# Performance work log

Hardware: AMD Instinct MI355X
Metric: run time of the kernel (lower is better)

The kernel has to match this reference:

```python
import jax, jax.numpy as jnp
import numpy as np
from jax import lax

BZ = 1024; ROI = 116; DIM = 116; FLAT = ROI * DIM
TOPK = 8; TEMP = 0.07; ALPHA = 0.1; A_COEF = 0.9; BETA = 2; EPS = 1e-5


def _leaky(v):
    return jnp.where(v >= 0, v, 0.2 * v)


def _bn2d(h, g, b):
    # training-mode BatchNorm1d on [N, C] (biased variance)
    m = h.mean(0)
    v = h.var(0)
    return (h - m) * lax.rsqrt(v + EPS) * g + b


def setup_inputs():
    key = jax.random.key(0)
    ks = jax.random.split(key, 16)
    def w(k, shape, s=0.05):
        return jax.random.normal(k, shape, jnp.float32) * s
    return {
        "x": jax.random.normal(ks[0], (BZ, ROI, DIM), jnp.float32),
        "pseudo": jax.random.normal(ks[1], (BZ, ROI, DIM), jnp.float32),
        "ages": jax.random.randint(ks[2], (BZ,), 0, 80, jnp.int32),
        "genders": jax.random.randint(ks[3], (BZ,), 0, 2, jnp.int32),
        "site": jax.random.randint(ks[4], (BZ, 4), 0, 10, jnp.int32),
        "fc_p_w": w(ks[5], (ROI, ROI)), "fc_p_b": jnp.zeros((ROI,), jnp.float32),
        "proj_w1": w(ks[6], (FLAT, ROI), 0.01), "proj_b1": jnp.zeros((ROI,), jnp.float32),
        "proj_w2": w(ks[7], (ROI, ROI)), "proj_b2": jnp.zeros((ROI,), jnp.float32),
        "gcn_w1": w(ks[8], (DIM, ROI)), "gcn_b1": jnp.zeros((ROI,), jnp.float32),
        "gcn_w2": w(ks[9], (ROI, ROI)), "gcn_b2": jnp.zeros((ROI,), jnp.float32),
        "gcn1_w": w(ks[10], (ROI, ROI)), "gcn1_b": jnp.zeros((ROI,), jnp.float32),
        "gcn2_w1": w(ks[11], (ROI, 64)), "gcn2_b1": jnp.zeros((64,), jnp.float32),
        "gcn2_w2": w(ks[12], (64, 8)), "gcn2_b2": jnp.zeros((8,), jnp.float32),
        "bn1_g": jnp.ones((ROI,), jnp.float32), "bn1_b": jnp.zeros((ROI,), jnp.float32),
        "bn2_g": jnp.ones((ROI,), jnp.float32), "bn2_b": jnp.zeros((ROI,), jnp.float32),
        "bn3_g": jnp.ones((ROI,), jnp.float32), "bn3_b": jnp.zeros((ROI,), jnp.float32),
    }


def _forward(x, pseudo, fc_p_w, fc_p_b, proj_w1, proj_b1, proj_w2, proj_b2,
             gcn_w1, gcn_b1, gcn_w2, gcn_b2, gcn1_w, gcn1_b,
             gcn2_w1, gcn2_b1, gcn2_w2, gcn2_b2,
             bn1_g, bn1_b, bn2_g, bn2_b, bn3_g, bn3_b,
             pos_idx, neg_idx, cond):
    bz = x.shape[0]
    pseudo = _leaky(pseudo @ fc_p_w + fc_p_b)
    x = x + pseudo                               # [bz, roi, dim]
    xf = x.reshape(bz, -1)                       # [bz, roi*dim]
    # contrastive head: Linear-ReLU-Linear, L2-normalize, cosine sim / temp
    p = jnp.maximum(xf @ proj_w1 + proj_b1, 0.0) @ proj_w2 + proj_b2
    pn = p / jnp.linalg.norm(p, axis=1, keepdims=True)
    sim = (pn @ pn.T) / TEMP                     # [bz, bz]
    sflat = sim.ravel()
    # -log(exp(pos)/(exp(pos)+exp(neg))) == softplus(neg - pos), truncated pairing
    loss = jnp.mean(jax.nn.softplus(sflat[neg_idx] - sflat[pos_idx]))
    sim_n = (sim - sim.min()) / (sim.max() - sim.min())
    # adjacency build: original does it in detached numpy -> stop_gradient
    xd = lax.stop_gradient(xf)
    sd = lax.stop_gradient(sim_n)
    sq = jnp.sum(xd * xd, axis=1)
    d2 = jnp.maximum(sq[:, None] + sq[None, :] - 2.0 * (xd @ xd.T), 0.0)
    fsim = jnp.exp(-ALPHA * jnp.sqrt(d2))
    total = fsim * (1.0 - sd) + sd
    dist = total * jnp.where(cond, A_COEF, 1.0 - A_COEF)
    vals, idxs = lax.top_k(dist, TOPK)           # row-wise top-8
    adj = jnp.zeros((bz, bz), jnp.float32).at[jnp.arange(bz)[:, None], idxs].set(vals)
    # GCN stack with flattened-feature message passing
    h = (adj @ xf).reshape(bz, ROI, DIM)
    h = _leaky(h @ gcn_w1 + gcn_b1) @ gcn_w2 + gcn_b2
    h = _bn2d(h.reshape(bz * ROI, -1), bn1_g, bn1_b).reshape(bz, ROI, -1)
    h = (adj @ h.reshape(bz, -1)).reshape(bz, ROI, -1)
    h = _leaky(h @ gcn1_w + gcn1_b)
    h = _bn2d(h.reshape(bz * ROI, -1), bn2_g, bn2_b).reshape(bz, ROI, -1)
    h = (adj @ h.reshape(bz, -1)).reshape(bz, ROI, -1)
    h = _leaky(_leaky(h @ gcn2_w1 + gcn2_b1) @ gcn2_w2 + gcn2_b2)  # [bz, roi, 8]
    # bn3: BatchNorm1d on [N, C=roi, L=8] -> per-channel over (N, L)
    m = h.mean((0, 2), keepdims=True)
    v = h.var((0, 2), keepdims=True)
    h = (h - m) * lax.rsqrt(v + EPS) * bn3_g[None, :, None] + bn3_b[None, :, None]
    return h, loss


def _masks(ages, genders, site):
    labels = np.asarray(site).argmax(1)
    eq = (labels[:, None] == labels[None, :]).ravel()
    pos_idx = np.nonzero(eq)[0]
    neg_idx = np.nonzero(~eq)[0]
    m = min(pos_idx.size, neg_idx.size)
    ag = np.asarray(ages); gd = np.asarray(genders)
    cond = (np.abs(ag[:, None] - ag[None, :]) <= BETA) & (gd[:, None] == gd[None, :])
    return jnp.asarray(pos_idx[:m]), jnp.asarray(neg_idx[:m]), jnp.asarray(cond)


def reference(x, pseudo, ages, genders, site, fc_p_w, fc_p_b, proj_w1, proj_b1,
              proj_w2, proj_b2, gcn_w1, gcn_b1, gcn_w2, gcn_b2, gcn1_w, gcn1_b,
              gcn2_w1, gcn2_b1, gcn2_w2, gcn2_b2, bn1_g, bn1_b, bn2_g, bn2_b,
              bn3_g, bn3_b):
    pos_idx, neg_idx, cond = _masks(ages, genders, site)
    return _forward(x, pseudo, fc_p_w, fc_p_b, proj_w1, proj_b1, proj_w2, proj_b2,
                    gcn_w1, gcn_b1, gcn_w2, gcn_b2, gcn1_w, gcn1_b,
                    gcn2_w1, gcn2_b1, gcn2_w2, gcn2_b2,
                    bn1_g, bn1_b, bn2_g, bn2_b, bn3_g, bn3_b,
                    pos_idx, neg_idx, cond)
```

## Files before the change

### kernel.cpp

```cpp
#include <hip/hip_runtime.h>
#include <math.h>

#define ROIN 116
#define NBZ 1024
#define LDF 128
#define SROW (ROIN*LDF)
#define NROWS (NBZ*ROIN)
#define ALPHA 0.1f
#define ACOEF 0.9f
#define BETAC 2
#define EPSBN 1e-5f
#define PZ 29
#define PCH 512
#define W1LD SROW
#define GX2 928
#define GX45 1856
#define GRAMZ 16
#define GRAMKS 928
#define NTRI 36

typedef __attribute__((ext_vector_type(8))) short bf16x8;
typedef __attribute__((ext_vector_type(4))) float f32x4;

__device__ __forceinline__ float leakyf(float v){ return v >= 0.f ? v : 0.2f*v; }

__device__ __forceinline__ short f2bf(float f){
    unsigned u = __builtin_bit_cast(unsigned, f);
    unsigned r = u + 0x7fffu + ((u >> 16) & 1u);
    return (short)(r >> 16);
}
__device__ __forceinline__ float bf2f(short h){
    unsigned u = ((unsigned)(unsigned short)h) << 16;
    return __builtin_bit_cast(float, u);
}

__global__ void wt_conv(const float* __restrict__ W, short* __restrict__ hi,
                        short* __restrict__ lo, int K, int N)
{
    int idx = blockIdx.x * 256 + threadIdx.x;
    int n = idx >> 7, k = idx & 127;
    float v = (n < N && k < K) ? W[(size_t)k * N + n] : 0.f;
    short h = f2bf(v);
    hi[idx] = h;
    lo[idx] = f2bf(v - bf2f(h));
}

__global__ void wt1_conv(const float* __restrict__ W, short* __restrict__ hi,
                         short* __restrict__ lo)
{
    int idx = blockIdx.x * 256 + threadIdx.x;
    int n = idx / W1LD, k = idx - n * W1LD;
    int r = k >> 7, d = k & 127;
    float v = (n < ROIN && d < ROIN) ? W[(size_t)(r * ROIN + d) * ROIN + n] : 0.f;
    short h = f2bf(v);
    hi[idx] = h;
    lo[idx] = f2bf(v - bf2f(h));
}

template<int EPI, int XTRA, bool PADK>
__global__ __launch_bounds__(512) void mfma_gemm_w(
    const float* __restrict__ A, const short* __restrict__ wt_hi,
    const short* __restrict__ wt_lo, const float* __restrict__ bias,
    const float* __restrict__ X, float* __restrict__ C,
    short* __restrict__ bfout, float* __restrict__ rsq, float* __restrict__ statp,
    int LDA, int LDC)
{
    __shared__ short whi[128][136];
    __shared__ short wlo[128][136];
    __shared__ float st[(XTRA == 2) ? 8 : 1][2][128];
    const int tid = threadIdx.x;
    {
        int r = tid >> 2, q = tid & 3;
        const short* sh = wt_hi + r * 128 + q * 32;
        const short* sl = wt_lo + r * 128 + q * 32;
        #pragma unroll
        for (int i = 0; i < 4; ++i) {
            *(bf16x8*)(&whi[r][q * 32 + i * 8]) = *(const bf16x8*)(sh + i * 8);
            *(bf16x8*)(&wlo[r][q * 32 + i * 8]) = *(const bf16x8*)(sl + i * 8);
        }
    }
    __syncthreads();
    const int wave = tid >> 6, lane = tid & 63;
    const int m0 = blockIdx.x * 128 + wave * 16;
    const int rl = lane & 15, g = lane >> 4;
    const float* Arow = A + (size_t)(m0 + rl) * LDA;
    float av[4][8];
    #pragma unroll
    for (int s = 0; s < 4; ++s) {
        const int kk = s * 32 + g * 8;
        if (PADK || kk + 8 <= ROIN) {
            float4 p = *(const float4*)(Arow + kk);
            float4 q = *(const float4*)(Arow + kk + 4);
            av[s][0]=p.x; av[s][1]=p.y; av[s][2]=p.z; av[s][3]=p.w;
            av[s][4]=q.x; av[s][5]=q.y; av[s][6]=q.z; av[s][7]=q.w;
        } else if (kk + 4 <= ROIN) {
            float4 p = *(const float4*)(Arow + kk);
            av[s][0]=p.x; av[s][1]=p.y; av[s][2]=p.z; av[s][3]=p.w;
            av[s][4]=0.f; av[s][5]=0.f; av[s][6]=0.f; av[s][7]=0.f;
        } else {
            #pragma unroll
            for (int j = 0; j < 8; ++j) av[s][j] = 0.f;
        }
    }
    f32x4 acc[8];
    #pragma unroll
    for (int nf = 0; nf < 8; ++nf) acc[nf] = (f32x4){0.f,0.f,0.f,0.f};
    #pragma unroll
    for (int s = 0; s < 4; ++s) {
        const int kk = s * 32 + g * 8;
        bf16x8 ah, al;
        #pragma unroll
        for (int j = 0; j < 8; ++j) {
            short h = f2bf(av[s][j]); ah[j] = h;
            al[j] = f2bf(av[s][j] - bf2f(h));
        }
        #pragma unroll
        for (int nf = 0; nf < 8; ++nf) {
            const bf16x8 bh = *(const bf16x8*)(&whi[nf * 16 + rl][kk]);
            const bf16x8 bl = *(const bf16x8*)(&wlo[nf * 16 + rl][kk]);
            acc[nf] = __builtin_amdgcn_mfma_f32_16x16x32_bf16(ah, bh, acc[nf], 0, 0, 0);
            acc[nf] = __builtin_amdgcn_mfma_f32_16x16x32_bf16(al, bh, acc[nf], 0, 0, 0);
            acc[nf] = __builtin_amdgcn_mfma_f32_16x16x32_bf16(ah, bl, acc[nf], 0, 0, 0);
        }
    }
    const int cm = g * 4;
    float rq[4] = {0.f, 0.f, 0.f, 0.f};
    bf16x8 bfv[4];
    #pragma unroll
    for (int nf = 0; nf < 8; ++nf) {
        int n = nf * 16 + rl;
        float c1 = 0.f, c2 = 0.f;
        float bb = (n < ROIN) ? bias[n] : 0.f;
        #pragma unroll
        for (int j = 0; j < 4; ++j) {
            int m = m0 + cm + j;
            size_t idx = (size_t)m * LDC + n;
            float v = 0.f;
            if (n < ROIN) {
                v = acc[nf][j] + bb;
                if (EPI == 3) v = leakyf(v);
                else if (EPI == 4) v = X[(size_t)m * LDA + n] + leakyf(v);
            }
            if (n < LDC) C[idx] = v;
            if (XTRA == 1) { bfv[j][nf] = f2bf(v); rq[j] += v * v; }
            if (XTRA == 2) { c1 += v; c2 += v * v; }
        }
        if (XTRA == 2) {
            c1 += __shfl_xor(c1, 16); c1 += __shfl_xor(c1, 32);
            c2 += __shfl_xor(c2, 16); c2 += __shfl_xor(c2, 32);
            if (lane < 16) { st[wave][0][n & 127] = c1; st[wave][1][n & 127] = c2; }
        }
    }
    if (XTRA == 1) {
        #pragma unroll
        for (int j = 0; j < 4; ++j)
            *(bf16x8*)(&bfout[(size_t)(m0 + cm + j) * LDF + rl * 8]) = bfv[j];
        #pragma unroll
        for (int j = 0; j < 4; ++j) {
            rq[j] += __shfl_xor(rq[j], 1);
            rq[j] += __shfl_xor(rq[j], 2);
            rq[j] += __shfl_xor(rq[j], 4);
            rq[j] += __shfl_xor(rq[j], 8);
        }
        if (rl == 0) {
            #pragma unroll
            for (int j = 0; j < 4; ++j) rsq[m0 + cm + j] = rq[j];
        }
    }
    if (XTRA == 2) {
        __syncthreads();
        if (tid < 232) {
            int sel = tid < 116 ? 0 : 1;
            int c = sel ? tid - 116 : tid;
            float s = 0.f;
            #pragma unroll
            for (int wv = 0; wv < 8; ++wv) s += st[wv][sel][c];
            statp[(size_t)(sel * 116 + c) * GX2 + blockIdx.x] = s;
        }
    }
}

template<int EPI, int XTRA, bool FOLD>
__global__ __launch_bounds__(512, 4) void mfma_gemm_wg(
    const float* __restrict__ vals, const int* __restrict__ idxs,
    const float* __restrict__ feat, const float* __restrict__ sb,
    const float* __restrict__ tb,
    const short* __restrict__ wt_hi, const short* __restrict__ wt_lo,
    const float* __restrict__ bias, float* __restrict__ C,
    float* __restrict__ statp)
{
    __shared__ short whi[128][136];
    __shared__ short wlo[128][136];
    __shared__ float st[(XTRA == 2) ? 8 : 1][2][128];
    const int tid = threadIdx.x;
    {
        int r = tid >> 2, q = tid & 3;
        const short* sh = wt_hi + r * 128 + q * 32;
        const short* sl = wt_lo + r * 128 + q * 32;
        #pragma unroll
        for (int i = 0; i < 4; ++i) {
            *(bf16x8*)(&whi[r][q * 32 + i * 8]) = *(const bf16x8*)(sh + i * 8);
            *(bf16x8*)(&wlo[r][q * 32 + i * 8]) = *(const bf16x8*)(sl + i * 8);
        }
    }
    __syncthreads();
    const int wave = tid >> 6, lane = tid & 63;
    const int m0 = blockIdx.x * 128 + wave * 16;
    const int rl = lane & 15, g = lane >> 4;
    const int m = m0 + rl;
    const unsigned bz = (unsigned)m / 116u;
    const int r = m - (int)bz * 116;
    float vv[8]; const float4* fp[8];
    #pragma unroll
    for (int k = 0; k < 8; ++k) {
        vv[k] = vals[bz * 8 + k];
        int ixk = idxs[bz * 8 + k];
        fp[k] = (const float4*)(feat + ((size_t)ixk * 116 + r) * 128);
    }
    float wsum = 0.f;
    if (FOLD) {
        #pragma unroll
        for (int k = 0; k < 8; ++k) wsum += vv[k];
    }
    f32x4 acc[8];
    #pragma unroll
    for (int nf = 0; nf < 8; ++nf) acc[nf] = (f32x4){0.f,0.f,0.f,0.f};
    float4 xp[8], xq[8];
    const int fb = g * 2;
    #pragma unroll
    for (int k = 0; k < 8; ++k) xp[k] = fp[k][fb];
    #pragma unroll
    for (int k = 0; k < 8; ++k) xq[k] = fp[k][fb + 1];
    #pragma unroll
    for (int s = 0; s < 4; ++s) {
        const int kk = s * 32 + g * 8;
        float4 P = {0.f,0.f,0.f,0.f}, Q = {0.f,0.f,0.f,0.f};
        #pragma unroll
        for (int k = 0; k < 8; ++k) {
            P.x = fmaf(vv[k], xp[k].x, P.x); P.y = fmaf(vv[k], xp[k].y, P.y);
            P.z = fmaf(vv[k], xp[k].z, P.z); P.w = fmaf(vv[k], xp[k].w, P.w);
            Q.x = fmaf(vv[k], xq[k].x, Q.x); Q.y = fmaf(vv[k], xq[k].y, Q.y);
            Q.z = fmaf(vv[k], xq[k].z, Q.z); Q.w = fmaf(vv[k], xq[k].w, Q.w);
        }
        if (s < 3) {
            const int fn = fb + (s + 1) * 8;
            #pragma unroll
            for (int k = 0; k < 8; ++k) xp[k] = fp[k][fn];
            #pragma unroll
            for (int k = 0; k < 8; ++k) xq[k] = fp[k][fn + 1];
        }
        float av[8] = {P.x, P.y, P.z, P.w, Q.x, Q.y, Q.z, Q.w};
        if (FOLD) {
            #pragma unroll
            for (int j = 0; j < 8; ++j) {
                int c = kk + j;
                av[j] = (c < ROIN) ? sb[c] * av[j] + wsum * tb[c] : 0.f;
            }
        }
        bf16x8 ah, al;
        #pragma unroll
        for (int j = 0; j < 8; ++j) {
            short h = f2bf(av[j]); ah[j] = h;
            al[j] = f2bf(av[j] - bf2f(h));
        }
        __builtin_amdgcn_s_setprio(1);
        #pragma unroll
        for (int nf = 0; nf < 8; ++nf) {
            const bf16x8 bh = *(const bf16x8*)(&whi[nf * 16 + rl][kk]);
            const bf16x8 bl = *(const bf16x8*)(&wlo[nf * 16 + rl][kk]);
            acc[nf] = __builtin_amdgcn_mfma_f32_16x16x32_bf16(ah, bh, acc[nf], 0, 0, 0);
            acc[nf] = __builtin_amdgcn_mfma_f32_16x16x32_bf16(al, bh, acc[nf], 0, 0, 0);
            acc[nf] = __builtin_amdgcn_mfma_f32_16x16x32_bf16(ah, bl, acc[nf], 0, 0, 0);
        }
        __builtin_amdgcn_s_setprio(0);
    }
    const int cm = g * 4;
    #pragma unroll
    for (int nf = 0; nf < 8; ++nf) {
        int n = nf * 16 + rl;
        float c1 = 0.f, c2 = 0.f;
        float bb = (n < ROIN) ? bias[n] : 0.f;
        #pragma unroll
        for (int j = 0; j < 4; ++j) {
            int mm = m0 + cm + j;
            float v = 0.f;
            if (n < ROIN) {
                v = acc[nf][j] + bb;
                if (EPI == 3) v = leakyf(v);
            }
            C[(size_t)mm * LDF + n] = v;
            if (XTRA == 2) { c1 += v; c2 += v * v; }
        }
        if (XTRA == 2) {
            c1 += __shfl_xor(c1, 16); c1 += __shfl_xor(c1, 32);
            c2 += __shfl_xor(c2, 16); c2 += __shfl_xor(c2, 32);
            if (lane < 16) { st[wave][0][n & 127] = c1; st[wave][1][n & 127] = c2; }
        }
    }
    if (XTRA == 2) {
        __syncthreads();
        if (tid < 232) {
            int sel = tid < 116 ? 0 : 1;
            int c = sel ? tid - 116 : tid;
            float s = 0.f;
            #pragma unroll
            for (int wv = 0; wv < 8; ++wv) s += st[wv][sel][c];
            statp[(size_t)(sel * 116 + c) * GX2 + blockIdx.x] = s;
        }
    }
}

__global__ __launch_bounds__(256) void mfma_gemm45_wg(
    const float* __restrict__ vals, const int* __restrict__ idxs,
    const float* __restrict__ feat, const float* __restrict__ sb,
    const float* __restrict__ tb,
    const short* __restrict__ w5h, const short* __restrict__ w5l,
    const float* __restrict__ b5,
    const short* __restrict__ w6h, const short* __restrict__ w6l,
    const float* __restrict__ b6,
    float* __restrict__ C)
{
    __shared__ short s5h[64][136], s5l[64][136];
    __shared__ short s6h[16][136], s6l[16][136];
    __shared__ float c1s[4][16][76];
    const int tid = threadIdx.x;
    {
        int r = tid >> 2, q = tid & 3;
        const short* sh = w5h + r * 128 + q * 32;
        const short* sl = w5l + r * 128 + q * 32;
        #pragma unroll
        for (int i = 0; i < 4; ++i) {
            *(bf16x8*)(&s5h[r][q * 32 + i * 8]) = *(const bf16x8*)(sh + i * 8);
            *(bf16x8*)(&s5l[r][q * 32 + i * 8]) = *(const bf16x8*)(sl + i * 8);
        }
        if (tid < 64) {
            int r6 = tid >> 2, q6 = tid & 3;
            const short* sh6 = w6h + r6 * 128 + q6 * 32;
            const short* sl6 = w6l + r6 * 128 + q6 * 32;
            #pragma unroll
            for (int i = 0; i < 4; ++i) {
                *(bf16x8*)(&s6h[r6][q6 * 32 + i * 8]) = *(const bf16x8*)(sh6 + i * 8);
                *(bf16x8*)(&s6l[r6][q6 * 32 + i * 8]) = *(const bf16x8*)(sl6 + i * 8);
            }
        }
    }
    __syncthreads();
    const int wave = tid >> 6, lane = tid & 63;
    const int m0 = blockIdx.x * 64 + wave * 16;
    const int rl = lane & 15, g = lane >> 4;
    const int m = m0 + rl;
    const unsigned bz = (unsigned)m / 116u;
    const int r = m - (int)bz * 116;
    float vv[8]; const float4* fp[8];
    #pragma unroll
    for (int k = 0; k < 8; ++k) {
        vv[k] = vals[bz * 8 + k];
        int ixk = idxs[bz * 8 + k];
        fp[k] = (const float4*)(feat + ((size_t)ixk * 116 + r) * 128);
    }
    float wsum = 0.f;
    #pragma unroll
    for (int k = 0; k < 8; ++k) wsum += vv[k];
    f32x4 acc[4];
    #pragma unroll
    for (int nf = 0; nf < 4; ++nf) acc[nf] = (f32x4){0.f,0.f,0.f,0.f};
    float4 xp[8], xq[8];
    const int fb = g * 2;
    #pragma unroll
    for (int k = 0; k < 8; ++k) xp[k] = fp[k][fb];
    #pragma unroll
    for (int k = 0; k < 8; ++k) xq[k] = fp[k][fb + 1];
    #pragma unroll
    for (int s = 0; s < 4; ++s) {
        const int kk = s * 32 + g * 8;
        float4 P = {0.f,0.f,0.f,0.f}, Q = {0.f,0.f,0.f,0.f};
        #pragma unroll
        for (int k = 0; k < 8; ++k) {
            P.x = fmaf(vv[k], xp[k].x, P.x); P.y = fmaf(vv[k], xp[k].y, P.y);
            P.z = fmaf(vv[k], xp[k].z, P.z); P.w = fmaf(vv[k], xp[k].w, P.w);
            Q.x = fmaf(vv[k], xq[k].x, Q.x); Q.y = fmaf(vv[k], xq[k].y, Q.y);
            Q.z = fmaf(vv[k], xq[k].z, Q.z); Q.w = fmaf(vv[k], xq[k].w, Q.w);
        }
        if (s < 3) {
            const int fn = fb + (s + 1) * 8;
            #pragma unroll
            for (int k = 0; k < 8; ++k) xp[k] = fp[k][fn];
            #pragma unroll
            for (int k = 0; k < 8; ++k) xq[k] = fp[k][fn + 1];
        }
        float av[8] = {P.x, P.y, P.z, P.w, Q.x, Q.y, Q.z, Q.w};
        #pragma unroll
        for (int j = 0; j < 8; ++j) {
            int c = kk + j;
            av[j] = (c < ROIN) ? sb[c] * av[j] + wsum * tb[c] : 0.f;
        }
        bf16x8 ah, al;
        #pragma unroll
        for (int j = 0; j < 8; ++j) {
            short h = f2bf(av[j]); ah[j] = h;
            al[j] = f2bf(av[j] - bf2f(h));
        }
        __builtin_amdgcn_s_setprio(1);
        #pragma unroll
        for (int nf = 0; nf < 4; ++nf) {
            const bf16x8 bh = *(const bf16x8*)(&s5h[nf * 16 + rl][kk]);
            const bf16x8 bl = *(const bf16x8*)(&s5l[nf * 16 + rl][kk]);
            acc[nf] = __builtin_amdgcn_mfma_f32_16x16x32_bf16(ah, bh, acc[nf], 0, 0, 0);
            acc[nf] = __builtin_amdgcn_mfma_f32_16x16x32_bf16(al, bh, acc[nf], 0, 0, 0);
            acc[nf] = __builtin_amdgcn_mfma_f32_16x16x32_bf16(ah, bl, acc[nf], 0, 0, 0);
        }
        __builtin_amdgcn_s_setprio(0);
    }
    const int cm = g * 4;
    #pragma unroll
    for (int nf = 0; nf < 4; ++nf) {
        int n = nf * 16 + rl;
        float bb = b5[n];
        #pragma unroll
        for (int j = 0; j < 4; ++j)
            c1s[wave][cm + j][n] = leakyf(acc[nf][j] + bb);
    }
    f32x4 acc2 = {0.f,0.f,0.f,0.f};
    #pragma unroll
    for (int s = 0; s < 2; ++s) {
        const int kk = s * 32 + g * 8;
        float4 p = *(const float4*)(&c1s[wave][rl][kk]);
        float4 q = *(const float4*)(&c1s[wave][rl][kk + 4]);
        float a2[8] = {p.x, p.y, p.z, p.w, q.x, q.y, q.z, q.w};
        bf16x8 ah, al;
        #pragma unroll
        for (int j = 0; j < 8; ++j) {
            short h = f2bf(a2[j]); ah[j] = h;
            al[j] = f2bf(a2[j] - bf2f(h));
        }
        const bf16x8 bh = *(const bf16x8*)(&s6h[rl][kk]);
        const bf16x8 bl = *(const bf16x8*)(&s6l[rl][kk]);
        acc2 = __builtin_amdgcn_mfma_f32_16x16x32_bf16(ah, bh, acc2, 0, 0, 0);
        acc2 = __builtin_amdgcn_mfma_f32_16x16x32_bf16(al, bh, acc2, 0, 0, 0);
        acc2 = __builtin_amdgcn_mfma_f32_16x16x32_bf16(ah, bl, acc2, 0, 0, 0);
    }
    if (rl < 8) {
        float bb = b6[rl];
        #pragma unroll
        for (int j = 0; j < 4; ++j) {
            float v = leakyf(acc2[j] + bb);
            C[(size_t)(m0 + cm + j) * 8 + rl] = v;
        }
    }
}

__global__ void bn_final_st(const float* __restrict__ statp, const float* __restrict__ g,
                            const float* __restrict__ bta, float* __restrict__ sb,
                            float* __restrict__ tb)
{
    int c = blockIdx.x, tid = threadIdx.x;
    float a1 = 0.f, a2 = 0.f;
    for (int i = tid; i < GX2; i += 256) {
        a1 += statp[(size_t)c * GX2 + i];
        a2 += statp[(size_t)(116 + c) * GX2 + i];
    }
    __shared__ float r1[256], r2[256];
    r1[tid] = a1; r2[tid] = a2; __syncthreads();
    for (int off = 128; off > 0; off >>= 1) {
        if (tid < off) { r1[tid] += r1[tid + off]; r2[tid] += r2[tid + off]; }
        __syncthreads();
    }
    if (tid == 0) {
        float mean = r1[0] / (float)NROWS;
        float var = r2[0] / (float)NROWS - mean * mean;
        float rstd = 1.f / sqrtf(var + EPSBN);
        float s = rstd * g[c];
        sb[c] = s;
        tb[c] = bta[c] - mean * s;
    }
}

__global__ void sq_reduce(const float* __restrict__ rsq, float* __restrict__ sq)
{
    int i = blockIdx.x * 256 + threadIdx.x;
    if (i >= NBZ) return;
    const float* p = rsq + (size_t)i * ROIN;
    float s = 0.f;
    #pragma unroll 4
    for (int r = 0; r < ROIN; ++r) s += p[r];
    sq[i] = s;
}

__global__ __launch_bounds__(256) void mfma_proj1(
    const float* __restrict__ A, const short* __restrict__ wt_hi,
    const short* __restrict__ wt_lo, float* __restrict__ part)
{
    const int wave = threadIdx.x >> 6, lane = threadIdx.x & 63;
    const int m0 = blockIdx.x * 64 + wave * 16;
    const int rl = lane & 15, g = lane >> 4;
    const int kbase = blockIdx.z * PCH;
    const float* Arow = A + (size_t)(m0 + rl) * SROW;
    f32x4 acc[8];
    #pragma unroll
    for (int nf = 0; nf < 8; ++nf) acc[nf] = (f32x4){0.f,0.f,0.f,0.f};
    for (int s = 0; s < 16; ++s) {
        const int kk = kbase + s * 32 + g * 8;
        float4 p = *(const float4*)(Arow + kk);
        float4 q = *(const float4*)(Arow + kk + 4);
        float av[8] = {p.x, p.y, p.z, p.w, q.x, q.y, q.z, q.w};
        bf16x8 ah, al;
        #pragma unroll
        for (int j = 0; j < 8; ++j) {
            short h = f2bf(av[j]); ah[j] = h;
            al[j] = f2bf(av[j] - bf2f(h));
        }
        #pragma unroll
        for (int nf = 0; nf < 8; ++nf) {
            size_t boff = (size_t)(nf * 16 + rl) * W1LD + kk;
            bf16x8 bh = *(const bf16x8*)(wt_hi + boff);
            bf16x8 bl = *(const bf16x8*)(wt_lo + boff);
            acc[nf] = __builtin_amdgcn_mfma_f32_16x16x32_bf16(ah, bh, acc[nf], 0, 0, 0);
            acc[nf] = __builtin_amdgcn_mfma_f32_16x16x32_bf16(al, bh, acc[nf], 0, 0, 0);
            acc[nf] = __builtin_amdgcn_mfma_f32_16x16x32_bf16(ah, bl, acc[nf], 0, 0, 0);
        }
    }
    float* Cb = part + (size_t)blockIdx.z * NBZ * ROIN;
    const int cm = g * 4;
    #pragma unroll
    for (int nf = 0; nf < 8; ++nf) {
        int n = nf * 16 + rl;
        if (n < ROIN) {
            #pragma unroll
            for (int j = 0; j < 4; ++j)
                Cb[(size_t)(m0 + cm + j) * ROIN + n] = acc[nf][j];
        }
    }
}

__global__ void proj_reduce(const float* __restrict__ ppart,
                            const float* __restrict__ bias, float* __restrict__ t1)
{
    int e = blockIdx.x * 256 + threadIdx.x;
    if (e >= NBZ * ROIN) return;
    int n = e % ROIN;
    float s = 0.f;
    for (int z = 0; z < PZ; ++z) s += ppart[(size_t)z * NBZ * ROIN + e];
    t1[e] = fmaxf(s + bias[n], 0.f);
}

__global__ __launch_bounds__(256) void gemm_nt_sym(
    const float* __restrict__ A, float* __restrict__ C, int M, int K, float scale)
{
    if ((int)blockIdx.y < (int)blockIdx.x) return;
    __shared__ float As[16][65];
    __shared__ float Bs[16][65];
    const int tid = threadIdx.x;
    const int m0 = blockIdx.x * 64;
    const int n0 = blockIdx.y * 64;
    const int tm4 = (tid >> 4) * 4;
    const int tn4 = (tid & 15) * 4;
    const int rA  = tid >> 2;
    const int kbA = (tid & 3) * 4;
    float acc[4][4] = {};
    for (int kt = 0; kt < K; kt += 16) {
        int kg = kt + kbA;
        if (kg + 4 <= K) {
            float4 va = *(const float4*)(A + (size_t)(m0 + rA) * K + kg);
            As[kbA + 0][rA] = va.x; As[kbA + 1][rA] = va.y;
            As[kbA + 2][rA] = va.z; As[kbA + 3][rA] = va.w;
            float4 vb = *(const float4*)(A + (size_t)(n0 + rA) * K + kg);
            Bs[kbA + 0][rA] = vb.x; Bs[kbA + 1][rA] = vb.y;
            Bs[kbA + 2][rA] = vb.z; Bs[kbA + 3][rA] = vb.w;
        } else {
            #pragma unroll
            for (int kk = 0; kk < 4; ++kk) {
                int kgg = kg + kk;
                As[kbA + kk][rA] = (kgg < K) ? A[(size_t)(m0 + rA) * K + kgg] : 0.f;
                Bs[kbA + kk][rA] = (kgg < K) ? A[(size_t)(n0 + rA) * K + kgg] : 0.f;
            }
        }
        __syncthreads();
        #pragma unroll
        for (int k = 0; k < 16; ++k) {
            float a[4], b[4];
            #pragma unroll
            for (int i = 0; i < 4; ++i) a[i] = As[k][tm4 + i];
            #pragma unroll
            for (int j = 0; j < 4; ++j) b[j] = Bs[k][tn4 + j];
            #pragma unroll
            for (int i = 0; i < 4; ++i)
                #pragma unroll
                for (int j = 0; j < 4; ++j)
                    acc[i][j] = fmaf(a[i], b[j], acc[i][j]);
        }
        __syncthreads();
    }
    #pragma unroll
    for (int i = 0; i < 4; ++i) {
        int m = m0 + tm4 + i;
        #pragma unroll
        for (int j = 0; j < 4; ++j) {
            int n = n0 + tn4 + j;
            float v = acc[i][j] * scale;
            C[(size_t)m * M + n] = v;
            C[(size_t)n * M + m] = v;
        }
    }
}

__global__ __launch_bounds__(256) void gram_mfma(
    const short* __restrict__ Xh, float* __restrict__ gpart)
{
    const int id = blockIdx.x;
    const int wg = (id & 7) * 72 + (id >> 3);
    const int z = wg / 36;
    const int tri = wg - z * 36;
    int bx = 0;
    #pragma unroll
    for (int b = 1; b < 8; ++b) {
        int base = b * 8 - (b * (b - 1)) / 2;
        if (base <= tri) bx = b;
    }
    const int by = tri - (bx * 8 - (bx * (bx - 1)) / 2) + bx;
    const int k0 = z * GRAMKS;
    const int wave = threadIdx.x >> 6, lane = threadIdx.x & 63;
    const int wr = wave >> 1, wc = wave & 1;
    const int row = lane & 15, koff = (lane >> 4) * 8;
    const short* Ap[4]; const short* Bp[4];
    #pragma unroll
    for (int i = 0; i < 4; ++i) {
        Ap[i] = Xh + (size_t)(bx * 128 + wr * 64 + i * 16 + row) * SROW;
// ... 204 lines not shown
        float v = sim[f];
        if (eq[kk]) { if (r < m) posval[r] = v; r++; }
        else { long nr = (long)f - r; if (nr < m) negval[nr] = v; }
    }
}

__global__ void loss_part(const float* __restrict__ posval, const float* __restrict__ negval,
                          const int* __restrict__ iscal, float* __restrict__ lp)
{
    int m = iscal[1];
    int t = threadIdx.x, b = blockIdx.x;
    float s = 0.f;
    for (int k = b * 256 + t; k < m; k += 1024 * 256) {
        float d = negval[k] - posval[k];
        s += fmaxf(d, 0.f) + log1pf(expf(-fabsf(d)));
    }
    __shared__ float red[256];
    red[t] = s; __syncthreads();
    for (int off = 128; off > 0; off >>= 1) { if (t < off) red[t] += red[t + off]; __syncthreads(); }
    if (t == 0) lp[b] = red[0];
}

__global__ void loss_final(const float* __restrict__ lp, const int* __restrict__ iscal,
                           float* __restrict__ outp)
{
    int t = threadIdx.x;
    double s = 0.0;
    for (int k = t; k < 1024; k += 256) s += (double)lp[k];
    __shared__ double red[256];
    red[t] = s; __syncthreads();
    for (int off = 128; off > 0; off >>= 1) { if (t < off) red[t] += red[t + off]; __syncthreads(); }
    if (t == 0) {
        int m = iscal[1]; if (m < 1) m = 1;
        outp[0] = (float)(red[0] / (double)m);
    }
}

__global__ void topk8(const float* __restrict__ dist, float* __restrict__ topv, int* __restrict__ topi)
{
    int row = blockIdx.x, t = threadIdx.x;
    __shared__ float sv[1024];
    __shared__ float rv[256];
    __shared__ int   ri[256];
    for (int j = t; j < 1024; j += 256) sv[j] = dist[(size_t)row * 1024 + j];
    __syncthreads();
    for (int k = 0; k < 8; ++k) {
        float bv = -1e30f; int bi = 1 << 20;
        for (int j = t; j < 1024; j += 256) {
            float x = sv[j];
            if (x > bv || (x == bv && j < bi)) { bv = x; bi = j; }
        }
        rv[t] = bv; ri[t] = bi;
        __syncthreads();
        for (int s = 128; s > 0; s >>= 1) {
            if (t < s) {
                float ov = rv[t + s]; int oi = ri[t + s];
                if (ov > rv[t] || (ov == rv[t] && oi < ri[t])) { rv[t] = ov; ri[t] = oi; }
            }
            __syncthreads();
        }
        if (t == 0) { topv[row * 8 + k] = rv[0]; topi[row * 8 + k] = ri[0]; sv[ri[0]] = -1e30f; }
        __syncthreads();
    }
}

__global__ void bn3_k(const float* __restrict__ X, const float* __restrict__ g,
                      const float* __restrict__ bta, float* __restrict__ out)
{
    int c = blockIdx.x, t = threadIdx.x;
    float s = 0.f, s2 = 0.f;
    for (int k = t; k < 8192; k += 256) {
        int n = k >> 3, l = k & 7;
        float v = X[(size_t)n * 928 + c * 8 + l];
        s += v; s2 += v * v;
    }
    __shared__ float rs[256], rs2[256];
    rs[t] = s; rs2[t] = s2; __syncthreads();
    for (int off = 128; off > 0; off >>= 1) {
        if (t < off) { rs[t] += rs[t + off]; rs2[t] += rs2[t + off]; }
        __syncthreads();
    }
    __shared__ float sm, sr;
    if (t == 0) {
        float mean = rs[0] / 8192.f;
        float var = rs2[0] / 8192.f - mean * mean;
        sm = mean; sr = 1.f / sqrtf(var + EPSBN);
    }
    __syncthreads();
    float mean = sm, rstd = sr, gg = g[c], bb = bta[c];
    for (int k = t; k < 8192; k += 256) {
        int n = k >> 3, l = k & 7;
        size_t idx = (size_t)n * 928 + c * 8 + l;
        out[idx] = (X[idx] - mean) * rstd * gg + bb;
    }
}

extern "C" void kernel_launch(void* const* d_in, const int* in_sizes, int n_in,
                              void* d_out, int out_size, void* d_ws, size_t ws_size,
                              hipStream_t stream)
{
    const float* x        = (const float*)d_in[0];
    const float* pseudo   = (const float*)d_in[1];
    const int*   ages     = (const int*)d_in[2];
    const int*   genders  = (const int*)d_in[3];
    const int*   site     = (const int*)d_in[4];
    const float* fc_p_w   = (const float*)d_in[5];
    const float* fc_p_b   = (const float*)d_in[6];
    const float* proj_w1  = (const float*)d_in[7];
    const float* proj_b1  = (const float*)d_in[8];
    const float* proj_w2  = (const float*)d_in[9];
    const float* proj_b2  = (const float*)d_in[10];
    const float* gcn_w1   = (const float*)d_in[11];
    const float* gcn_b1   = (const float*)d_in[12];
    const float* gcn_w2   = (const float*)d_in[13];
    const float* gcn_b2   = (const float*)d_in[14];
    const float* gcn1_w   = (const float*)d_in[15];
    const float* gcn1_b   = (const float*)d_in[16];
    const float* gcn2_w1  = (const float*)d_in[17];
    const float* gcn2_b1  = (const float*)d_in[18];
    const float* gcn2_w2  = (const float*)d_in[19];
    const float* gcn2_b2  = (const float*)d_in[20];
    const float* bn1_g    = (const float*)d_in[21];
    const float* bn1_b    = (const float*)d_in[22];
    const float* bn2_g    = (const float*)d_in[23];
    const float* bn2_b    = (const float*)d_in[24];
    const float* bn3_g    = (const float*)d_in[25];
    const float* bn3_b    = (const float*)d_in[26];
    float* dout = (float*)d_out;

    char* w = (char*)d_ws;
    size_t off = 0;
    auto carve = [&](size_t bytes) { char* p = w + off; off = (off + bytes + 255) & ~(size_t)255; return p; };
    float* xf     = (float*)carve((size_t)NROWS * LDF * 4);
    float* hA     = (float*)carve((size_t)NROWS * LDF * 4);
    float* hB     = (float*)carve((size_t)NROWS * LDF * 4);
    float* G      = (float*)carve(1048576u * 4);
    float* simb   = (float*)carve(1048576u * 4);
    float* t1     = (float*)carve((size_t)NBZ * ROIN * 4);
    float* pbuf   = (float*)carve((size_t)NBZ * ROIN * 4);
    float* sq     = (float*)carve(4096);
    float* rsq    = (float*)carve((size_t)NROWS * 4);
    int*   labels = (int*)carve(4096);
    int*   rowcnt = (int*)carve(4096);
    int*   rowoff = (int*)carve(4096);
    int*   iscal  = (int*)carve(256);
    float* fscal  = (float*)carve(256);
    float* posval = (float*)carve(524288u * 4);
    float* negval = (float*)carve(524288u * 4);
    float* lpart  = (float*)carve(4096);
    float* mmpart = (float*)carve(4096);
    float* topv   = (float*)carve(32768);
    int*   topi   = (int*)carve(32768);
    float* statp  = (float*)carve((size_t)232 * GX2 * 4);
    float* sbA    = (float*)carve(512);
    float* tbA    = (float*)carve(512);
    float* sbB    = (float*)carve(512);
    float* tbB    = (float*)carve(512);
    short* wt1_hi = (short*)carve((size_t)128 * W1LD * 2);
    short* wt1_lo = (short*)carve((size_t)128 * W1LD * 2);
    short* wts    = (short*)carve((size_t)7 * 2 * 16384 * 2);
    float* ppart  = hA;
    float* gpart  = hA;
    short* xfh    = (short*)((char*)hB + (16u << 20));

    auto wt_hi = [&](int i) { return wts + (size_t)i * 2 * 16384; };
    auto wt_lo = [&](int i) { return wts + (size_t)i * 2 * 16384 + 16384; };

    wt1_conv<<<(128 * W1LD) / 256, 256, 0, stream>>>(proj_w1, wt1_hi, wt1_lo);
    wt_conv<<<64, 256, 0, stream>>>(fc_p_w,   wt_hi(0), wt_lo(0), 116, 116);
    wt_conv<<<64, 256, 0, stream>>>(proj_w2,  wt_hi(1), wt_lo(1), 116, 116);
    wt_conv<<<64, 256, 0, stream>>>(gcn_w1,   wt_hi(2), wt_lo(2), 116, 116);
    wt_conv<<<64, 256, 0, stream>>>(gcn_w2,   wt_hi(3), wt_lo(3), 116, 116);
    wt_conv<<<64, 256, 0, stream>>>(gcn1_w,   wt_hi(4), wt_lo(4), 116, 116);
    wt_conv<<<64, 256, 0, stream>>>(gcn2_w1,  wt_hi(5), wt_lo(5), 116, 64);
    wt_conv<<<64, 256, 0, stream>>>(gcn2_w2,  wt_hi(6), wt_lo(6), 64, 8);

    mfma_gemm_w<4, 1, false><<<GX2, 512, 0, stream>>>(pseudo, wt_hi(0), wt_lo(0), fc_p_b, x, xf,
                                                      xfh, rsq, nullptr, ROIN, LDF);
    sq_reduce<<<4, 256, 0, stream>>>(rsq, sq);

    mfma_proj1<<<dim3(16, 1, PZ), 256, 0, stream>>>(xf, wt1_hi, wt1_lo, ppart);
    proj_reduce<<<(NBZ * ROIN + 255) / 256, 256, 0, stream>>>(ppart, proj_b1, t1);
    mfma_gemm_w<1, 0, false><<<8, 512, 0, stream>>>(t1, wt_hi(1), wt_lo(1), proj_b2, nullptr, pbuf,
                                                    nullptr, nullptr, nullptr, ROIN, ROIN);
    rownorm<<<NBZ, 128, 0, stream>>>(pbuf);

    gemm_nt_sym<<<dim3(16, 16, 1), 256, 0, stream>>>(pbuf, simb, NBZ, ROIN, 1.f / 0.07f);

    labels_k<<<4, 256, 0, stream>>>(site, labels);
    rowcnt_k<<<4, 256, 0, stream>>>(labels, rowcnt);
    scan_k<<<1, 1024, 0, stream>>>(rowcnt, rowoff, iscal);
    pair_scatter<<<NBZ, 256, 0, stream>>>(labels, rowoff, iscal, simb, posval, negval);
    loss_part<<<1024, 256, 0, stream>>>(posval, negval, iscal, lpart);
    loss_final<<<1, 256, 0, stream>>>(lpart, iscal, dout + (size_t)NBZ * ROIN * 8);

    minmax_part<<<512, 256, 0, stream>>>(simb, mmpart);
    minmax_final<<<1, 512, 0, stream>>>(mmpart, fscal);
    gram_mfma<<<NTRI * GRAMZ, 256, 0, stream>>>(xfh, gpart);
    gram_reduce_dist<<<dim3(NTRI, 16), 256, 0, stream>>>(gpart, simb, sq, ages, genders, fscal, G);
    topk8<<<NBZ, 256, 0, stream>>>(G, topv, topi);

    mfma_gemm_wg<3, 0, false><<<GX2, 512, 0, stream>>>(topv, topi, xf, nullptr, nullptr,
                                                       wt_hi(2), wt_lo(2), gcn_b1, hB, nullptr);
    mfma_gemm_w<1, 2, true><<<GX2, 512, 0, stream>>>(hB, wt_hi(3), wt_lo(3), gcn_b2, nullptr, hA,
                                                     nullptr, nullptr, statp, LDF, LDF);
    bn_final_st<<<116, 256, 0, stream>>>(statp, bn1_g, bn1_b, sbA, tbA);

    mfma_gemm_wg<3, 2, true><<<GX2, 512, 0, stream>>>(topv, topi, hA, sbA, tbA,
                                                      wt_hi(4), wt_lo(4), gcn1_b, hB, statp);
    bn_final_st<<<116, 256, 0, stream>>>(statp, bn2_g, bn2_b, sbB, tbB);

    mfma_gemm45_wg<<<GX45, 256, 0, stream>>>(topv, topi, hB, sbB, tbB,
                                             wt_hi(5), wt_lo(5), gcn2_b1,
                                             wt_hi(6), wt_lo(6), gcn2_b2, hA);

    bn3_k<<<116, 256, 0, stream>>>(hA, bn3_g, bn3_b, dout);
}
```

Before: 685.9 us.

## Store GCN intermediate activations in bf16 with permuted K layout

Switches the GCN-stage activations (xf copy, gcn outputs, BN-folded inputs) from fp32 to single bf16 storage, which halves the gathered top-k neighbor traffic. The weights are permuted along K so that contiguous bf16x8 loads match the MFMA fragment order, and the BN scale/shift vectors are written in that same permuted order. A new bf16-input GEMM drops the lo-part of the activation split, so it needs two MFMAs instead of three. The trade is lower precision in the intermediate activations, which could hurt accuracy against the reference.

```diff
diff --git a/kernel.cpp b/kernel.cpp
--- a/kernel.cpp
+++ b/kernel.cpp
@@ -34,11 +34,14 @@
     return __builtin_bit_cast(float, u);
 }
 
+
+template<bool PERM>
 __global__ void wt_conv(const float* __restrict__ W, short* __restrict__ hi,
                         short* __restrict__ lo, int K, int N)
 {
     int idx = blockIdx.x * 256 + threadIdx.x;
-    int n = idx >> 7, k = idx & 127;
+    int n = idx >> 7, kp = idx & 127;
+    int k = PERM ? ((kp & 7) * 16 + (kp >> 3)) : kp;
     float v = (n < N && k < K) ? W[(size_t)k * N + n] : 0.f;
     short h = f2bf(v);
     hi[idx] = h;
@@ -62,12 +65,11 @@
     const float* __restrict__ A, const short* __restrict__ wt_hi,
     const short* __restrict__ wt_lo, const float* __restrict__ bias,
     const float* __restrict__ X, float* __restrict__ C,
-    short* __restrict__ bfout, float* __restrict__ rsq, float* __restrict__ statp,
+    short* __restrict__ bfout, float* __restrict__ rsq,
     int LDA, int LDC)
 {
     __shared__ short whi[128][136];
     __shared__ short wlo[128][136];
-    __shared__ float st[(XTRA == 2) ? 8 : 1][2][128];
     const int tid = threadIdx.x;
     {
         int r = tid >> 2, q = tid & 3;
@@ -129,7 +131,6 @@
     #pragma unroll
     for (int nf = 0; nf < 8; ++nf) {
         int n = nf * 16 + rl;
-        float c1 = 0.f, c2 = 0.f;
         float bb = (n < ROIN) ? bias[n] : 0.f;
         #pragma unroll
         for (int j = 0; j < 4; ++j) {
@@ -143,12 +144,6 @@
             }
             if (n < LDC) C[idx] = v;
             if (XTRA == 1) { bfv[j][nf] = f2bf(v); rq[j] += v * v; }
-            if (XTRA == 2) { c1 += v; c2 += v * v; }
-        }
-        if (XTRA == 2) {
-            c1 += __shfl_xor(c1, 16); c1 += __shfl_xor(c1, 32);
-            c2 += __shfl_xor(c2, 16); c2 += __shfl_xor(c2, 32);
-            if (lane < 16) { st[wave][0][n & 127] = c1; st[wave][1][n & 127] = c2; }
         }
     }
     if (XTRA == 1) {
@@ -167,26 +162,15 @@
             for (int j = 0; j < 4; ++j) rsq[m0 + cm + j] = rq[j];
         }
     }
-    if (XTRA == 2) {
-        __syncthreads();
-        if (tid < 232) {
-            int sel = tid < 116 ? 0 : 1;
-            int c = sel ? tid - 116 : tid;
-            float s = 0.f;
-            #pragma unroll
-            for (int wv = 0; wv < 8; ++wv) s += st[wv][sel][c];
-            statp[(size_t)(sel * 116 + c) * GX2 + blockIdx.x] = s;
-        }
-    }
-}
-
-template<int EPI, int XTRA, bool FOLD>
-__global__ __launch_bounds__(512, 4) void mfma_gemm_wg(
+}
+
+template<int XTRA, bool FOLD>
+__global__ __launch_bounds__(512, 4) void mfma_gemm_wg_h(
     const float* __restrict__ vals, const int* __restrict__ idxs,
-    const float* __restrict__ feat, const float* __restrict__ sb,
-    const float* __restrict__ tb,
+    const short* __restrict__ feat, const float* __restrict__ sbP,
+    const float* __restrict__ tbP,
     const short* __restrict__ wt_hi, const short* __restrict__ wt_lo,
-    const float* __restrict__ bias, float* __restrict__ C,
+    const float* __restrict__ bias, short* __restrict__ outH,
     float* __restrict__ statp)
 {
     __shared__ short whi[128][136];
@@ -210,12 +194,12 @@
     const int m = m0 + rl;
     const unsigned bz = (unsigned)m / 116u;
     const int r = m - (int)bz * 116;
-    float vv[8]; const float4* fp[8];
+    float vv[8]; const short* fp[8];
     #pragma unroll
     for (int k = 0; k < 8; ++k) {
         vv[k] = vals[bz * 8 + k];
         int ixk = idxs[bz * 8 + k];
-        fp[k] = (const float4*)(feat + ((size_t)ixk * 116 + r) * 128);
+        fp[k] = feat + ((size_t)ixk * 116 + r) * 128;
     }
     float wsum = 0.f;
     if (FOLD) {
@@ -225,37 +209,27 @@
     f32x4 acc[8];
     #pragma unroll
     for (int nf = 0; nf < 8; ++nf) acc[nf] = (f32x4){0.f,0.f,0.f,0.f};
-    float4 xp[8], xq[8];
-    const int fb = g * 2;
-    #pragma unroll
-    for (int k = 0; k < 8; ++k) xp[k] = fp[k][fb];
-    #pragma unroll
-    for (int k = 0; k < 8; ++k) xq[k] = fp[k][fb + 1];
+    bf16x8 xb[8], xn[8];
+    #pragma unroll
+    for (int k = 0; k < 8; ++k) xb[k] = *(const bf16x8*)(fp[k] + g * 8);
     #pragma unroll
     for (int s = 0; s < 4; ++s) {
         const int kk = s * 32 + g * 8;
-        float4 P = {0.f,0.f,0.f,0.f}, Q = {0.f,0.f,0.f,0.f};
+        if (s < 3) {
+            #pragma unroll
+            for (int k = 0; k < 8; ++k) xn[k] = *(const bf16x8*)(fp[k] + kk + 32);
+        }
+        float av[8] = {0.f,0.f,0.f,0.f,0.f,0.f,0.f,0.f};
         #pragma unroll
         for (int k = 0; k < 8; ++k) {
-            P.x = fmaf(vv[k], xp[k].x, P.x); P.y = fmaf(vv[k], xp[k].y, P.y);
-            P.z = fmaf(vv[k], xp[k].z, P.z); P.w = fmaf(vv[k], xp[k].w, P.w);
-            Q.x = fmaf(vv[k], xq[k].x, Q.x); Q.y = fmaf(vv[k], xq[k].y, Q.y);
-            Q.z = fmaf(vv[k], xq[k].z, Q.z); Q.w = fmaf(vv[k], xq[k].w, Q.w);
-        }
-        if (s < 3) {
-            const int fn = fb + (s + 1) * 8;
-            #pragma unroll
-            for (int k = 0; k < 8; ++k) xp[k] = fp[k][fn];
-            #pragma unroll
-            for (int k = 0; k < 8; ++k) xq[k] = fp[k][fn + 1];
-        }
-        float av[8] = {P.x, P.y, P.z, P.w, Q.x, Q.y, Q.z, Q.w};
+            const float vk = vv[k];
+            #pragma unroll
+            for (int j = 0; j < 8; ++j) av[j] = fmaf(vk, bf2f(xb[k][j]), av[j]);
+        }
         if (FOLD) {
             #pragma unroll
-            for (int j = 0; j < 8; ++j) {
-                int c = kk + j;
-                av[j] = (c < ROIN) ? sb[c] * av[j] + wsum * tb[c] : 0.f;
-            }
+            for (int j = 0; j < 8; ++j)
+                av[j] = sbP[kk + j] * av[j] + wsum * tbP[kk + j];
         }
         bf16x8 ah, al;
         #pragma unroll
@@ -273,8 +247,11 @@
             acc[nf] = __builtin_amdgcn_mfma_f32_16x16x32_bf16(ah, bl, acc[nf], 0, 0, 0);
         }
         __builtin_amdgcn_s_setprio(0);
+        #pragma unroll
+        for (int k = 0; k < 8; ++k) xb[k] = xn[k];
     }
     const int cm = g * 4;
+    bf16x8 bfv[4];
     #pragma unroll
     for (int nf = 0; nf < 8; ++nf) {
         int n = nf * 16 + rl;
@@ -282,13 +259,9 @@
         float bb = (n < ROIN) ? bias[n] : 0.f;
         #pragma unroll
         for (int j = 0; j < 4; ++j) {
-            int mm = m0 + cm + j;
             float v = 0.f;
-            if (n < ROIN) {
-                v = acc[nf][j] + bb;
-                if (EPI == 3) v = leakyf(v);
-            }
-            C[(size_t)mm * LDF + n] = v;
+            if (n < ROIN) v = leakyf(acc[nf][j] + bb);
+            bfv[j][nf] = f2bf(v);
             if (XTRA == 2) { c1 += v; c2 += v * v; }
         }
         if (XTRA == 2) {
@@ -297,6 +270,9 @@
             if (lane < 16) { st[wave][0][n & 127] = c1; st[wave][1][n & 127] = c2; }
         }
     }
+    #pragma unroll
+    for (int j = 0; j < 4; ++j)
+        *(bf16x8*)(&outH[(size_t)(m0 + cm + j) * LDF + rl * 8]) = bfv[j];
     if (XTRA == 2) {
         __syncthreads();
         if (tid < 232) {
@@ -310,10 +286,85 @@
     }
 }
 
-__global__ __launch_bounds__(256) void mfma_gemm45_wg(
+__global__ __launch_bounds__(512) void mfma_gemm_bA(
+    const short* __restrict__ A,
+    const short* __restrict__ wt_hi, const short* __restrict__ wt_lo,
+    const float* __restrict__ bias, short* __restrict__ outH,
+    float* __restrict__ statp)
+{
+    __shared__ short whi[128][136];
+    __shared__ short wlo[128][136];
+    __shared__ float st[8][2][128];
+    const int tid = threadIdx.x;
+    {
+        int r = tid >> 2, q = tid & 3;
+        const short* sh = wt_hi + r * 128 + q * 32;
+        const short* sl = wt_lo + r * 128 + q * 32;
+        #pragma unroll
+        for (int i = 0; i < 4; ++i) {
+            *(bf16x8*)(&whi[r][q * 32 + i * 8]) = *(const bf16x8*)(sh + i * 8);
+            *(bf16x8*)(&wlo[r][q * 32 + i * 8]) = *(const bf16x8*)(sl + i * 8);
+        }
+    }
+    __syncthreads();
+    const int wave = tid >> 6, lane = tid & 63;
+    const int m0 = blockIdx.x * 128 + wave * 16;
+    const int rl = lane & 15, g = lane >> 4;
+    const short* Arow = A + (size_t)(m0 + rl) * LDF;
+    bf16x8 av[4];
+    #pragma unroll
+    for (int s = 0; s < 4; ++s) av[s] = *(const bf16x8*)(Arow + s * 32 + g * 8);
+    f32x4 acc[8];
+    #pragma unroll
+    for (int nf = 0; nf < 8; ++nf) acc[nf] = (f32x4){0.f,0.f,0.f,0.f};
+    #pragma unroll
+    for (int s = 0; s < 4; ++s) {
+        const int kk = s * 32 + g * 8;
+        const bf16x8 ah = av[s];
+        #pragma unroll
+        for (int nf = 0; nf < 8; ++nf) {
+            const bf16x8 bh = *(const bf16x8*)(&whi[nf * 16 + rl][kk]);
+            const bf16x8 bl = *(const bf16x8*)(&wlo[nf * 16 + rl][kk]);
+            acc[nf] = __builtin_amdgcn_mfma_f32_16x16x32_bf16(ah, bh, acc[nf], 0, 0, 0);
+            acc[nf] = __builtin_amdgcn_mfma_f32_16x16x32_bf16(ah, bl, acc[nf], 0, 0, 0);
+        }
+    }
+    const int cm = g * 4;
+    bf16x8 bfv[4];
+    #pragma unroll
+    for (int nf = 0; nf < 8; ++nf) {
+        int n = nf * 16 + rl;
+        float c1 = 0.f, c2 = 0.f;
+        float bb = (n < ROIN) ? bias[n] : 0.f;
+        #pragma unroll
+        for (int j = 0; j < 4; ++j) {
+            float v = 0.f;
+            if (n < ROIN) v = acc[nf][j] + bb;
+            bfv[j][nf] = f2bf(v);
+            c1 += v; c2 += v * v;
+        }
+        c1 += __shfl_xor(c1, 16); c1 += __shfl_xor(c1, 32);
+        c2 += __shfl_xor(c2, 16); c2 += __shfl_xor(c2, 32);
+        if (lane < 16) { st[wave][0][n & 127] = c1; st[wave][1][n & 127] = c2; }
+    }
+    #pragma unroll
+    for (int j = 0; j < 4; ++j)
+        *(bf16x8*)(&outH[(size_t)(m0 + cm + j) * LDF + rl * 8]) = bfv[j];
+    __syncthreads();
+    if (tid < 232) {
+        int sel = tid < 116 ? 0 : 1;
+        int c = sel ? tid - 116 : tid;
+        float s = 0.f;
+        #pragma unroll
+        for (int wv = 0; wv < 8; ++wv) s += st[wv][sel][c];
+        statp[(size_t)(sel * 116 + c) * GX2 + blockIdx.x] = s;
+    }
+}
+
+__global__ __launch_bounds__(256) void mfma_gemm45_wg_h(
     const float* __restrict__ vals, const int* __restrict__ idxs,
-    const float* __restrict__ feat, const float* __restrict__ sb,
-    const float* __restrict__ tb,
+    const short* __restrict__ feat, const float* __restrict__ sbP,
+    const float* __restrict__ tbP,
     const short* __restrict__ w5h, const short* __restrict__ w5l,
     const float* __restrict__ b5,
     const short* __restrict__ w6h, const short* __restrict__ w6l,
@@ -351,12 +402,12 @@
     const int m = m0 + rl;
     const unsigned bz = (unsigned)m / 116u;
     const int r = m - (int)bz * 116;
-    float vv[8]; const float4* fp[8];
+    float vv[8]; const short* fp[8];
     #pragma unroll
     for (int k = 0; k < 8; ++k) {
         vv[k] = vals[bz * 8 + k];
         int ixk = idxs[bz * 8 + k];
-        fp[k] = (const float4*)(feat + ((size_t)ixk * 116 + r) * 128);
+        fp[k] = feat + ((size_t)ixk * 116 + r) * 128;
     }
     float wsum = 0.f;
     #pragma unroll
@@ -364,36 +415,26 @@
     f32x4 acc[4];
     #pragma unroll
     for (int nf = 0; nf < 4; ++nf) acc[nf] = (f32x4){0.f,0.f,0.f,0.f};
-    float4 xp[8], xq[8];
-    const int fb = g * 2;
-    #pragma unroll
-    for (int k = 0; k < 8; ++k) xp[k] = fp[k][fb];
-    #pragma unroll
-    for (int k = 0; k < 8; ++k) xq[k] = fp[k][fb + 1];
+    bf16x8 xb[8], xn[8];
+    #pragma unroll
+    for (int k = 0; k < 8; ++k) xb[k] = *(const bf16x8*)(fp[k] + g * 8);
     #pragma unroll
     for (int s = 0; s < 4; ++s) {
         const int kk = s * 32 + g * 8;
-        float4 P = {0.f,0.f,0.f,0.f}, Q = {0.f,0.f,0.f,0.f};
+        if (s < 3) {
+            #pragma unroll
+            for (int k = 0; k < 8; ++k) xn[k] = *(const bf16x8*)(fp[k] + kk + 32);
+        }
+        float av[8] = {0.f,0.f,0.f,0.f,0.f,0.f,0.f,0.f};
         #pragma unroll
         for (int k = 0; k < 8; ++k) {
-            P.x = fmaf(vv[k], xp[k].x, P.x); P.y = fmaf(vv[k], xp[k].y, P.y);
-            P.z = fmaf(vv[k], xp[k].z, P.z); P.w = fmaf(vv[k], xp[k].w, P.w);
-            Q.x = fmaf(vv[k], xq[k].x, Q.x); Q.y = fmaf(vv[k], xq[k].y, Q.y);
-            Q.z = fmaf(vv[k], xq[k].z, Q.z); Q.w = fmaf(vv[k], xq[k].w, Q.w);
-        }
-        if (s < 3) {
-            const int fn = fb + (s + 1) * 8;
-            #pragma unroll
-            for (int k = 0; k < 8; ++k) xp[k] = fp[k][fn];
-            #pragma unroll
-            for (int k = 0; k < 8; ++k) xq[k] = fp[k][fn + 1];
-        }
-        float av[8] = {P.x, P.y, P.z, P.w, Q.x, Q.y, Q.z, Q.w};
-        #pragma unroll
-        for (int j = 0; j < 8; ++j) {
-            int c = kk + j;
-            av[j] = (c < ROIN) ? sb[c] * av[j] + wsum * tb[c] : 0.f;
-        }
+            const float vk = vv[k];
+            #pragma unroll
+            for (int j = 0; j < 8; ++j) av[j] = fmaf(vk, bf2f(xb[k][j]), av[j]);
+        }
+        #pragma unroll
+        for (int j = 0; j < 8; ++j)
+            av[j] = sbP[kk + j] * av[j] + wsum * tbP[kk + j];
         bf16x8 ah, al;
         #pragma unroll
         for (int j = 0; j < 8; ++j) {
@@ -410,6 +451,8 @@
             acc[nf] = __builtin_amdgcn_mfma_f32_16x16x32_bf16(ah, bl, acc[nf], 0, 0, 0);
         }
         __builtin_amdgcn_s_setprio(0);
+        #pragma unroll
+        for (int k = 0; k < 8; ++k) xb[k] = xn[k];
     }
     const int cm = g * 4;
     #pragma unroll
@@ -449,15 +492,17 @@
     }
 }
 
-__global__ void bn_final_st(const float* __restrict__ statp, const float* __restrict__ g,
-                            const float* __restrict__ bta, float* __restrict__ sb,
-                            float* __restrict__ tb)
+__global__ void bn_final_st_p(const float* __restrict__ statp, const float* __restrict__ g,
+                              const float* __restrict__ bta, float* __restrict__ sbP,
+                              float* __restrict__ tbP, int cnt)
 {
     int c = blockIdx.x, tid = threadIdx.x;
+    int pc = (c & 15) * 8 + (c >> 4);
+    if (c >= ROIN) { if (tid == 0) { sbP[pc] = 0.f; tbP[pc] = 0.f; } return; }
     float a1 = 0.f, a2 = 0.f;
-    for (int i = tid; i < GX2; i += 256) {
-        a1 += statp[(size_t)c * GX2 + i];
-        a2 += statp[(size_t)(116 + c) * GX2 + i];
+    for (int i = tid; i < cnt; i += 256) {
+        a1 += statp[(size_t)c * cnt + i];
+        a2 += statp[(size_t)(116 + c) * cnt + i];
     }
     __shared__ float r1[256], r2[256];
     r1[tid] = a1; r2[tid] = a2; __syncthreads();
@@ -470,8 +515,8 @@
         float var = r2[0] / (float)NROWS - mean * mean;
         float rstd = 1.f / sqrtf(var + EPSBN);
         float s = rstd * g[c];
-        sb[c] = s;
-        tb[c] = bta[c] - mean * s;
+        sbP[pc] = s;
+        tbP[pc] = bta[c] - mean * s;
     }
 }
 
@@ -982,37 +1027,41 @@
     float* topv   = (float*)carve(32768);
     int*   topi   = (int*)carve(32768);
     float* statp  = (float*)carve((size_t)232 * GX2 * 4);
-    float* sbA    = (float*)carve(512);
-    float* tbA    = (float*)carve(512);
-    float* sbB    = (float*)carve(512);
-    float* tbB    = (float*)carve(512);
+    float* sbAp   = (float*)carve(512);
+    float* tbAp   = (float*)carve(512);
+    float* sbBp   = (float*)carve(512);
+    float* tbBp   = (float*)carve(512);
     short* wt1_hi = (short*)carve((size_t)128 * W1LD * 2);
     short* wt1_lo = (short*)carve((size_t)128 * W1LD * 2);
     short* wts    = (short*)carve((size_t)7 * 2 * 16384 * 2);
     float* ppart  = hA;
     float* gpart  = hA;
     short* xfh    = (short*)((char*)hB + (16u << 20));
+    short* actH1  = (short*)hA;
+    short* actH2  = (short*)hB;
+    short* actH3  = (short*)hA;
+    float* h45    = hB;
 
     auto wt_hi = [&](int i) { return wts + (size_t)i * 2 * 16384; };
     auto wt_lo = [&](int i) { return wts + (size_t)i * 2 * 16384 + 16384; };
 
     wt1_conv<<<(128 * W1LD) / 256, 256, 0, stream>>>(proj_w1, wt1_hi, wt1_lo);
-    wt_conv<<<64, 256, 0, stream>>>(fc_p_w,   wt_hi(0), wt_lo(0), 116, 116);
-    wt_conv<<<64, 256, 0, stream>>>(proj_w2,  wt_hi(1), wt_lo(1), 116, 116);
-    wt_conv<<<64, 256, 0, stream>>>(gcn_w1,   wt_hi(2), wt_lo(2), 116, 116);
-    wt_conv<<<64, 256, 0, stream>>>(gcn_w2,   wt_hi(3), wt_lo(3), 116, 116);
-    wt_conv<<<64, 256, 0, stream>>>(gcn1_w,   wt_hi(4), wt_lo(4), 116, 116);
-    wt_conv<<<64, 256, 0, stream>>>(gcn2_w1,  wt_hi(5), wt_lo(5), 116, 64);
-    wt_conv<<<64, 256, 0, stream>>>(gcn2_w2,  wt_hi(6), wt_lo(6), 64, 8);
+    wt_conv<false><<<64, 256, 0, stream>>>(fc_p_w,  wt_hi(0), wt_lo(0), 116, 116);
+    wt_conv<false><<<64, 256, 0, stream>>>(proj_w2, wt_hi(1), wt_lo(1), 116, 116);
+    wt_conv<true ><<<64, 256, 0, stream>>>(gcn_w1,  wt_hi(2), wt_lo(2), 116, 116);
+    wt_conv<true ><<<64, 256, 0, stream>>>(gcn_w2,  wt_hi(3), wt_lo(3), 116, 116);
+    wt_conv<true ><<<64, 256, 0, stream>>>(gcn1_w,  wt_hi(4), wt_lo(4), 116, 116);
+    wt_conv<true ><<<64, 256, 0, stream>>>(gcn2_w1, wt_hi(5), wt_lo(5), 116, 64);
+    wt_conv<false><<<64, 256, 0, stream>>>(gcn2_w2, wt_hi(6), wt_lo(6), 64, 8);
 
     mfma_gemm_w<4, 1, false><<<GX2, 512, 0, stream>>>(pseudo, wt_hi(0), wt_lo(0), fc_p_b, x, xf,
-                                                      xfh, rsq, nullptr, ROIN, LDF);
+                                                      xfh, rsq, ROIN, LDF);
     sq_reduce<<<4, 256, 0, stream>>>(rsq, sq);
 
     mfma_proj1<<<dim3(16, 1, PZ), 256, 0, stream>>>(xf, wt1_hi, wt1_lo, ppart);
     proj_reduce<<<(NBZ * ROIN + 255) / 256, 256, 0, stream>>>(ppart, proj_b1, t1);
     mfma_gemm_w<1, 0, false><<<8, 512, 0, stream>>>(t1, wt_hi(1), wt_lo(1), proj_b2, nullptr, pbuf,
-                                                    nullptr, nullptr, nullptr, ROIN, ROIN);
+                                                    nullptr, nullptr, ROIN, ROIN);
     rownorm<<<NBZ, 128, 0, stream>>>(pbuf);
 
     gemm_nt_sym<<<dim3(16, 16, 1), 256, 0, stream>>>(pbuf, simb, NBZ, ROIN, 1.f / 0.07f);
@@ -1030,19 +1079,18 @@
     gram_reduce_dist<<<dim3(NTRI, 16), 256, 0, stream>>>(gpart, simb, sq, ages, genders, fscal, G);
     topk8<<<NBZ, 256, 0, stream>>>(G, topv, topi);
 
-    mfma_gemm_wg<3, 0, false><<<GX2, 512, 0, stream>>>(topv, topi, xf, nullptr, nullptr,
-                                                       wt_hi(2), wt_lo(2), gcn_b1, hB, nullptr);
-    mfma_gemm_w<1, 2, true><<<GX2, 512, 0, stream>>>(hB, wt_hi(3), wt_lo(3), gcn_b2, nullptr, hA,
-                                                     nullptr, nullptr, statp, LDF, LDF);
-    bn_final_st<<<116, 256, 0, stream>>>(statp, bn1_g, bn1_b, sbA, tbA);
-
-    mfma_gemm_wg<3, 2, true><<<GX2, 512, 0, stream>>>(topv, topi, hA, sbA, tbA,
-                                                      wt_hi(4), wt_lo(4), gcn1_b, hB, statp);
-    bn_final_st<<<116, 256, 0, stream>>>(statp, bn2_g, bn2_b, sbB, tbB);
-
-    mfma_gemm45_wg<<<GX45, 256, 0, stream>>>(topv, topi, hB, sbB, tbB,
-                                             wt_hi(5), wt_lo(5), gcn2_b1,
-                                             wt_hi(6), wt_lo(6), gcn2_b2, hA);
-
-    bn3_k<<<116, 256, 0, stream>>>(hA, bn3_g, bn3_b, dout);
-}
+    mfma_gemm_wg_h<0, false><<<GX2, 512, 0, stream>>>(topv, topi, xfh, nullptr, nullptr,
+                                                      wt_hi(2), wt_lo(2), gcn_b1, actH1, nullptr);
+    mfma_gemm_bA<<<GX2, 512, 0, stream>>>(actH1, wt_hi(3), wt_lo(3), gcn_b2, actH2, statp);
+    bn_final_st_p<<<128, 256, 0, stream>>>(statp, bn1_g, bn1_b, sbAp, tbAp, GX2);
+
+    mfma_gemm_wg_h<2, true><<<GX2, 512, 0, stream>>>(topv, topi, actH2, sbAp, tbAp,
+                                                     wt_hi(4), wt_lo(4), gcn1_b, actH3, statp);
+    bn_final_st_p<<<128, 256, 0, stream>>>(statp, bn2_g, bn2_b, sbBp, tbBp, GX2);
+
+    mfma_gemm45_wg_h<<<GX45, 256, 0, stream>>>(topv, topi, actH3, sbBp, tbBp,
+                                               wt_hi(5), wt_lo(5), gcn2_b1,
+                                               wt_hi(6), wt_lo(6), gcn2_b2, h45);
+
+    bn3_k<<<116, 256, 0, stream>>>(h45, bn3_g, bn3_b, dout);
+}
```

New measurement: 588.4 us, median of 2. 1.17x faster.
